# Performance work log

Measured on AMD Instinct MI355X. Metric: run time of the kernel, lower is better.

## Reference

```python
import jax, jax.numpy as jnp
import numpy as np

N_NODES = 100000
N_EDGES = 1600000


def sgconv(x, src, dst, W, b, K=1):
    """PyG SGConv: K hops of GCN-normalized propagation, then Linear."""
    n = x.shape[0]
    # add self loops
    loop = jnp.arange(n, dtype=src.dtype)
    s = jnp.concatenate([src, loop])  # source (j)
    d = jnp.concatenate([dst, loop])  # target (i)
    # symmetric normalization: deg over targets of A+I
    deg = jax.ops.segment_sum(jnp.ones_like(d, dtype=x.dtype), d, num_segments=n)
    dinv = jnp.where(deg > 0, jax.lax.rsqrt(deg), 0.0)
    norm = dinv[s] * dinv[d]  # [E+N]
    for _ in range(K):
        msg = x[s] * norm[:, None]  # gather + scale  [E+N, F]
        x = jax.ops.segment_sum(msg, d, num_segments=n)  # scatter-add
    return x @ W + b


def setup_inputs() -> dict:
    key = jax.random.key(0)
    k1, k2, k3, k4, k5, k6, k7 = jax.random.split(key, 7)
    x = jax.random.normal(k1, (N_NODES, 128), dtype=jnp.float32)
    edge_index = jax.random.randint(k2, (2, N_EDGES), 0, N_NODES, dtype=jnp.int64)
    # Glorot-ish scaled weights
    W1 = jax.random.normal(k3, (128, 128), dtype=jnp.float32) * (1.0 / np.sqrt(128))
    b1 = jax.random.normal(k4, (128,), dtype=jnp.float32) * 0.01
    W2 = jax.random.normal(k5, (128, 64), dtype=jnp.float32) * (1.0 / np.sqrt(128))
    b2 = jax.random.normal(k6, (64,), dtype=jnp.float32) * 0.01
    return {"x": x, "edge_index": edge_index, "W1": W1, "b1": b1, "W2": W2, "b2": b2}


def reference(x, edge_index, W1, b1, W2, b2):
    src, dst = edge_index[0], edge_index[1]
    h = sgconv(x, src, dst, W1, b1, K=1)
    out = sgconv(h, src, dst, W2, b2, K=1)
    return out
```

## Files before the change

### kernel.cpp

```cpp
#include <hip/hip_runtime.h>

#define NN 100000
#define NE 1600000
#define BSH 9
#define NPB (1 << BSH)
#define NBKT ((NN + NPB - 1) >> BSH)
#define ABLK 400
#define EPB (NE / ABLK)
#define CAP 10240

typedef __attribute__((ext_vector_type(8))) short short8;
typedef __attribute__((ext_vector_type(4))) float f32x4;

__device__ __forceinline__ unsigned short bf16r(float f) {
    unsigned u = __float_as_uint(f);
    u += 0x7fffu + ((u >> 16) & 1u);
    return (unsigned short)(u >> 16);
}
__device__ __forceinline__ unsigned pack2(float a, float b) {
    unsigned ua = __float_as_uint(a), ub = __float_as_uint(b);
    ua += 0x7fffu + ((ua >> 16) & 1u);
    ub += 0x7fffu + ((ub >> 16) & 1u);
    return (ua >> 16) | (ub & 0xffff0000u);
}
__device__ __forceinline__ float2 unpack2(unsigned u) {
    float2 r;
    r.x = __uint_as_float(u << 16);
    r.y = __uint_as_float(u & 0xffff0000u);
    return r;
}

__global__ __launch_bounds__(256) void k_scat2(const int* __restrict__ src,
                                               const int* __restrict__ dst,
                                               unsigned* __restrict__ cur,
                                               unsigned* __restrict__ epk) {
    __shared__ unsigned hcnt[NBKT];
    __shared__ unsigned hbase[NBKT];
    int b = blockIdx.x, t = threadIdx.x;
    for (int k = t; k < NBKT; k += 256) hcnt[k] = 0;
    __syncthreads();
    int e0 = b * EPB;
    for (int e = e0 + t; e < e0 + EPB; e += 256)
        atomicAdd(&hcnt[(unsigned)dst[e] >> BSH], 1u);
    __syncthreads();
    for (int k = t; k < NBKT; k += 256) {
        unsigned c = hcnt[k];
        hbase[k] = k * CAP + (c ? atomicAdd(&cur[k], c) : 0u);
        hcnt[k] = 0;
    }
    __syncthreads();
    for (int e = e0 + t; e < e0 + EPB; e += 256) {
        unsigned d = (unsigned)dst[e];
        unsigned kb = d >> BSH;
        unsigned pos = hbase[kb] + atomicAdd(&hcnt[kb], 1u);
        epk[pos] = ((d & (NPB - 1)) << 17) | (unsigned)src[e];
    }
}

__global__ __launch_bounds__(512) void k_csrB2(const unsigned* __restrict__ cur,
                                               const unsigned* __restrict__ epk,
                                               int* __restrict__ csr, int* __restrict__ off,
                                               int* __restrict__ deg, float* __restrict__ dinv,
                                               const float* __restrict__ W1,
                                               const float* __restrict__ W2,
                                               const float* __restrict__ b1,
                                               unsigned short* __restrict__ W12b,
                                               float* __restrict__ c2) {
    int blk = blockIdx.x;
    if (blk >= NBKT) {
        int idx = (blk - NBKT) * 512 + threadIdx.x;
        if (idx < 8192) {
            int i = idx >> 6, j = idx & 63;
            float acc = 0.f;
            for (int k = 0; k < 128; ++k) acc += W1[i * 128 + k] * W2[k * 64 + j];
            W12b[j * 128 + i] = bf16r(acc);
        } else if (idx < 8192 + 64) {
            int j = idx - 8192;
            float acc = 0.f;
            for (int k = 0; k < 128; ++k) acc += b1[k] * W2[k * 64 + j];
            c2[j] = acc;
        }
        return;
    }
    __shared__ unsigned lcnt[NPB];
    __shared__ unsigned lcur[NPB];
    int k = blk, t = threadIdx.x;
    unsigned e0 = (unsigned)k * CAP, e1 = e0 + cur[k];
    lcnt[t] = 0;
    __syncthreads();
    for (unsigned e = e0 + t; e < e1; e += NPB)
        atomicAdd(&lcnt[epk[e] >> 17], 1u);
    __syncthreads();
    unsigned own = lcnt[t];
    lcur[t] = own;
    __syncthreads();
    for (int d = 1; d < NPB; d <<= 1) {
        unsigned v = (t >= d) ? lcur[t - d] : 0;
        __syncthreads();
        lcur[t] += v;
        __syncthreads();
    }
    unsigned excl = lcur[t] - own;
    int n = k * NPB + t;
    if (n < NN) {
        off[n]  = (int)(e0 + excl);
        deg[n]  = (int)own;
        dinv[n] = rsqrtf((float)own + 1.0f);
    }
    __syncthreads();
    lcur[t] = excl;
    __syncthreads();
    for (unsigned e = e0 + t; e < e1; e += NPB) {
        unsigned u = epk[e];
        unsigned pos = atomicAdd(&lcur[u >> 17], 1u);
        csr[e0 + pos] = (int)(u & 0x1FFFFu);
    }
}

__global__ __launch_bounds__(256) void k_gemmYs(const float* __restrict__ x,
                                                const unsigned short* __restrict__ W12b,
                                                const float* __restrict__ dinv,
                                                unsigned short* __restrict__ ys) {
    __shared__ float Al[64][132];
    __shared__ short Wl[64][136];
    int t = threadIdx.x;
    int row0 = blockIdx.x * 64;

    for (int idx8 = t; idx8 < 1024; idx8 += 256) {
        int n = idx8 >> 4, c8 = idx8 & 15;
        *(short8*)&Wl[n][c8 * 8] = *(const short8*)&W12b[n * 128 + c8 * 8];
    }
    for (int idx = t; idx < 64 * 32; idx += 256) {
        int r = idx >> 5, c4 = idx & 31;
        float4 v = make_float4(0.f, 0.f, 0.f, 0.f);
        if (row0 + r < NN) v = *(const float4*)&x[(size_t)(row0 + r) * 128 + c4 * 4];
        *(float4*)&Al[r][c4 * 4] = v;
    }
    __syncthreads();

    int wv = t >> 6, lane = t & 63;
    int l15 = lane & 15, l4 = lane >> 4;

    short8 afr[4];
    #pragma unroll
    for (int ks = 0; ks < 4; ++ks) {
        const float* ap = &Al[wv * 16 + l15][ks * 32 + l4 * 8];
        float4 f0 = *(const float4*)ap;
        float4 f1 = *(const float4*)(ap + 4);
        short8 a;
        a[0] = (short)bf16r(f0.x); a[1] = (short)bf16r(f0.y);
        a[2] = (short)bf16r(f0.z); a[3] = (short)bf16r(f0.w);
        a[4] = (short)bf16r(f1.x); a[5] = (short)bf16r(f1.y);
        a[6] = (short)bf16r(f1.z); a[7] = (short)bf16r(f1.w);
        afr[ks] = a;
    }
    short8 bfr[4][4];
    #pragma unroll
    for (int ct = 0; ct < 4; ++ct)
        #pragma unroll
        for (int ks = 0; ks < 4; ++ks)
            bfr[ct][ks] = *(const short8*)&Wl[ct * 16 + l15][ks * 32 + l4 * 8];

    f32x4 acc[4] = {};
    #pragma unroll
    for (int ks = 0; ks < 4; ++ks)
        #pragma unroll
        for (int ct = 0; ct < 4; ++ct)
            acc[ct] = __builtin_amdgcn_mfma_f32_16x16x32_bf16(afr[ks], bfr[ct][ks], acc[ct], 0, 0, 0);

    int rbase = row0 + wv * 16 + l4 * 4;
    float di[4];
    #pragma unroll
    for (int r = 0; r < 4; ++r) di[r] = (rbase + r < NN) ? dinv[rbase + r] : 0.f;
    #pragma unroll
    for (int ct = 0; ct < 4; ++ct) {
        int col = ct * 16 + l15;
        #pragma unroll
        for (int r = 0; r < 4; ++r) {
            if (rbase + r < NN)
                ys[(size_t)(rbase + r) * 64 + col] = bf16r(acc[ct][r] * di[r]);
        }
    }
}

__global__ __launch_bounds__(256) void k_gatherA(const int* __restrict__ off,
        const int* __restrict__ deg, const int* __restrict__ csr,
        const float* __restrict__ dinv, const uint2* __restrict__ ys,
        const float* __restrict__ c2, uint2* __restrict__ ts) {
    int gid = blockIdx.x * blockDim.x + threadIdx.x;
    int node = gid >> 4;
    int lane = threadIdx.x & 15;
    if (node >= NN) return;
    uint2 u = ys[(size_t)node * 16 + lane];
    float2 a = unpack2(u.x), b = unpack2(u.y);
    float ax = a.x, ay = a.y, az = b.x, aw = b.y;
    int e = off[node], end = e + deg[node];
    for (; e + 8 <= end; e += 8) {
        uint2 uu[8];
        #pragma unroll
        for (int j = 0; j < 8; ++j) uu[j] = ys[(size_t)csr[e + j] * 16 + lane];
        #pragma unroll
        for (int j = 0; j < 8; ++j) {
            float2 t = unpack2(uu[j].x); ax += t.x; ay += t.y;
            t = unpack2(uu[j].y); az += t.x; aw += t.y;
        }
    }
    for (; e + 4 <= end; e += 4) {
        uint2 uu[4];
        #pragma unroll
        for (int j = 0; j < 4; ++j) uu[j] = ys[(size_t)csr[e + j] * 16 + lane];
        #pragma unroll
        for (int j = 0; j < 4; ++j) {
            float2 t = unpack2(uu[j].x); ax += t.x; ay += t.y;
            t = unpack2(uu[j].y); az += t.x; aw += t.y;
        }
    }
    for (; e < end; ++e) {
        uint2 uu = ys[(size_t)csr[e] * 16 + lane];
        float2 t = unpack2(uu.x); ax += t.x; ay += t.y;
        t = unpack2(uu.y); az += t.x; aw += t.y;
    }
    float di = dinv[node];
    float s = di * di;
    float4 cc = ((const float4*)c2)[lane];
    ts[(size_t)node * 16 + lane] = make_uint2(pack2(s * ax + di * cc.x, s * ay + di * cc.y),
                                              pack2(s * az + di * cc.z, s * aw + di * cc.w));
}

__global__ __launch_bounds__(256) void k_gatherB(const int* __restrict__ off,
        const int* __restrict__ deg, const int* __restrict__ csr,
        const float* __restrict__ dinv, const uint2* __restrict__ ts,
        const float* __restrict__ bias, float4* __restrict__ out) {
    int gid = blockIdx.x * blockDim.x + threadIdx.x;
    int node = gid >> 4;
    int lane = threadIdx.x & 15;
    if (node >= NN) return;
    uint2 u = ts[(size_t)node * 16 + lane];
    float2 a = unpack2(u.x), b = unpack2(u.y);
    float ax = a.x, ay = a.y, az = b.x, aw = b.y;
    int e = off[node], end = e + deg[node];
    for (; e + 8 <= end; e += 8) {
        uint2 uu[8];
        #pragma unroll
        for (int j = 0; j < 8; ++j) uu[j] = ts[(size_t)csr[e + j] * 16 + lane];
        #pragma unroll
        for (int j = 0; j < 8; ++j) {
            float2 t = unpack2(uu[j].x); ax += t.x; ay += t.y;
            t = unpack2(uu[j].y); az += t.x; aw += t.y;
        }
    }
    for (; e + 4 <= end; e += 4) {
        uint2 uu[4];
        #pragma unroll
        for (int j = 0; j < 4; ++j) uu[j] = ts[(size_t)csr[e + j] * 16 + lane];
        #pragma unroll
        for (int j = 0; j < 4; ++j) {
            float2 t = unpack2(uu[j].x); ax += t.x; ay += t.y;
            t = unpack2(uu[j].y); az += t.x; aw += t.y;
        }
    }
    for (; e < end; ++e) {
        uint2 uu = ts[(size_t)csr[e] * 16 + lane];
        float2 t = unpack2(uu.x); ax += t.x; ay += t.y;
        t = unpack2(uu.y); az += t.x; aw += t.y;
    }
    float di = dinv[node];
    float4 bb = ((const float4*)bias)[lane];
    out[(size_t)node * 16 + lane] = make_float4(ax * di + bb.x, ay * di + bb.y,
                                                az * di + bb.z, aw * di + bb.w);
}

extern "C" void kernel_launch(void* const* d_in, const int* in_sizes, int n_in,
                              void* d_out, int out_size, void* d_ws, size_t ws_size,
                              hipStream_t stream) {
    const float* x  = (const float*)d_in[0];
    const int*   ei = (const int*)d_in[1];
    const float* W1 = (const float*)d_in[2];
    const float* b1 = (const float*)d_in[3];
    const float* W2 = (const float*)d_in[4];
    const float* b2 = (const float*)d_in[5];
    float* out = (float*)d_out;

    const int* src = ei;
    const int* dst = ei + NE;

    float* fws  = (float*)d_ws;
    float* dinv = fws;
    unsigned* ys = (unsigned*)(fws + 102400);
    unsigned* ts = ys + (size_t)NN * 32;
    unsigned short* W12b = (unsigned short*)(ts + (size_t)NN * 32);
    float* c2   = (float*)(W12b + 8192);
    int* off  = (int*)(c2 + 128);
    int* deg  = off + 100096;
    int* csr  = deg + 100096;
    unsigned* epk = (unsigned*)(csr + NBKT * CAP);
    unsigned* cur = epk + NBKT * CAP;

    hipMemsetAsync(cur, 0, NBKT * sizeof(unsigned), stream);
    k_scat2<<<ABLK, 256, 0, stream>>>(src, dst, cur, epk);
    k_csrB2<<<NBKT + 17, 512, 0, stream>>>(cur, epk, csr, off, deg, dinv,
                                           W1, W2, b1, W12b, c2);

    k_gemmYs<<<(NN + 63) / 64, 256, 0, stream>>>(x, W12b, dinv, (unsigned short*)ys);

    k_gatherA<<<(NN * 16 + 255) / 256, 256, 0, stream>>>(off, deg, csr, dinv,
                                                         (const uint2*)ys, c2, (uint2*)ts);

    k_gatherB<<<(NN * 16 + 255) / 256, 256, 0, stream>>>(off, deg, csr, dinv,
                                                         (const uint2*)ts, b2, (float4*)out);
}
```

Before: 138.6 us.

## Merge CSR build into one cooperative kernel and widen gather loads to 16 bytes

A single cooperative kernel now does the memset, the weight-product precompute, the bucket scatter and the per-bucket CSR build, with grid-wide syncs in place of separate launches. This removes two launches and a memset. The gather kernels now use 8 lanes per node with uint4 (16-byte) loads of bf16 rows instead of 16 lanes with uint2, which halves the number of load instructions per neighbour. In exchange the CSR build runs on only 256 blocks and pays grid-sync cost, and the gathers run fewer threads, giving less parallelism to hide latency.

After: 195.7 us. 1.41x slower.

```diff
diff --git a/kernel.cpp b/kernel.cpp
--- a/kernel.cpp
+++ b/kernel.cpp
@@ -1,12 +1,15 @@
 #include <hip/hip_runtime.h>
+#include <hip/hip_cooperative_groups.h>
+
+namespace cg = cooperative_groups;
 
 #define NN 100000
 #define NE 1600000
 #define BSH 9
 #define NPB (1 << BSH)
 #define NBKT ((NN + NPB - 1) >> BSH)
-#define ABLK 400
-#define EPB (NE / ABLK)
+#define CBLK 256
+#define CEPB (NE / CBLK)
 #define CAP 10240
 
 typedef __attribute__((ext_vector_type(8))) short short8;
@@ -30,90 +33,86 @@
     return r;
 }
 
-__global__ __launch_bounds__(256) void k_scat2(const int* __restrict__ src,
-                                               const int* __restrict__ dst,
-                                               unsigned* __restrict__ cur,
-                                               unsigned* __restrict__ epk) {
-    __shared__ unsigned hcnt[NBKT];
-    __shared__ unsigned hbase[NBKT];
-    int b = blockIdx.x, t = threadIdx.x;
-    for (int k = t; k < NBKT; k += 256) hcnt[k] = 0;
+__global__ __launch_bounds__(512) void k_coop_csr(
+        const int* __restrict__ src, const int* __restrict__ dst,
+        unsigned* __restrict__ cur, unsigned* __restrict__ epk,
+        int* __restrict__ csr, int* __restrict__ off,
+        int* __restrict__ deg, float* __restrict__ dinv,
+        const float* __restrict__ W1, const float* __restrict__ W2,
+        const float* __restrict__ b1, unsigned short* __restrict__ W12b,
+        float* __restrict__ c2) {
+    cg::grid_group grid = cg::this_grid();
+    __shared__ unsigned sA[512];
+    __shared__ unsigned sB[512];
+    const int b = blockIdx.x, t = threadIdx.x;
+    const int gid = b * 512 + t;
+
+    if (gid < 8192) {
+        int i = gid >> 6, j = gid & 63;
+        float acc = 0.f;
+        for (int k = 0; k < 128; ++k) acc += W1[i * 128 + k] * W2[k * 64 + j];
+        W12b[j * 128 + i] = bf16r(acc);
+    } else if (gid < 8192 + 64) {
+        int j = gid - 8192;
+        float acc = 0.f;
+        for (int k = 0; k < 128; ++k) acc += b1[k] * W2[k * 64 + j];
+        c2[j] = acc;
+    } else if (gid - 8256 < NBKT && gid >= 8256) {
+        cur[gid - 8256] = 0u;
+    }
+    grid.sync();
+
+    for (int k = t; k < NBKT; k += 512) sA[k] = 0;
     __syncthreads();
-    int e0 = b * EPB;
-    for (int e = e0 + t; e < e0 + EPB; e += 256)
-        atomicAdd(&hcnt[(unsigned)dst[e] >> BSH], 1u);
+    const int e0 = b * CEPB;
+    for (int e = e0 + t; e < e0 + CEPB; e += 512)
+        atomicAdd(&sA[(unsigned)dst[e] >> BSH], 1u);
     __syncthreads();
-    for (int k = t; k < NBKT; k += 256) {
-        unsigned c = hcnt[k];
-        hbase[k] = k * CAP + (c ? atomicAdd(&cur[k], c) : 0u);
-        hcnt[k] = 0;
+    for (int k = t; k < NBKT; k += 512) {
+        unsigned c = sA[k];
+        sB[k] = k * CAP + (c ? atomicAdd(&cur[k], c) : 0u);
+        sA[k] = 0;
     }
     __syncthreads();
-    for (int e = e0 + t; e < e0 + EPB; e += 256) {
+    for (int e = e0 + t; e < e0 + CEPB; e += 512) {
         unsigned d = (unsigned)dst[e];
         unsigned kb = d >> BSH;
-        unsigned pos = hbase[kb] + atomicAdd(&hcnt[kb], 1u);
+        unsigned pos = sB[kb] + atomicAdd(&sA[kb], 1u);
         epk[pos] = ((d & (NPB - 1)) << 17) | (unsigned)src[e];
     }
-}
-
-__global__ __launch_bounds__(512) void k_csrB2(const unsigned* __restrict__ cur,
-                                               const unsigned* __restrict__ epk,
-                                               int* __restrict__ csr, int* __restrict__ off,
-                                               int* __restrict__ deg, float* __restrict__ dinv,
-                                               const float* __restrict__ W1,
-                                               const float* __restrict__ W2,
-                                               const float* __restrict__ b1,
-                                               unsigned short* __restrict__ W12b,
-                                               float* __restrict__ c2) {
-    int blk = blockIdx.x;
-    if (blk >= NBKT) {
-        int idx = (blk - NBKT) * 512 + threadIdx.x;
-        if (idx < 8192) {
-            int i = idx >> 6, j = idx & 63;
-            float acc = 0.f;
-            for (int k = 0; k < 128; ++k) acc += W1[i * 128 + k] * W2[k * 64 + j];
-            W12b[j * 128 + i] = bf16r(acc);
-        } else if (idx < 8192 + 64) {
-            int j = idx - 8192;
-            float acc = 0.f;
-            for (int k = 0; k < 128; ++k) acc += b1[k] * W2[k * 64 + j];
-            c2[j] = acc;
-        }
-        return;
-    }
-    __shared__ unsigned lcnt[NPB];
-    __shared__ unsigned lcur[NPB];
-    int k = blk, t = threadIdx.x;
-    unsigned e0 = (unsigned)k * CAP, e1 = e0 + cur[k];
-    lcnt[t] = 0;
-    __syncthreads();
-    for (unsigned e = e0 + t; e < e1; e += NPB)
-        atomicAdd(&lcnt[epk[e] >> 17], 1u);
-    __syncthreads();
-    unsigned own = lcnt[t];
-    lcur[t] = own;
-    __syncthreads();
-    for (int d = 1; d < NPB; d <<= 1) {
-        unsigned v = (t >= d) ? lcur[t - d] : 0;
-        __syncthreads();
-        lcur[t] += v;
-        __syncthreads();
-    }
-    unsigned excl = lcur[t] - own;
-    int n = k * NPB + t;
-    if (n < NN) {
-        off[n]  = (int)(e0 + excl);
-        deg[n]  = (int)own;
-        dinv[n] = rsqrtf((float)own + 1.0f);
-    }
-    __syncthreads();
-    lcur[t] = excl;
-    __syncthreads();
-    for (unsigned e = e0 + t; e < e1; e += NPB) {
-        unsigned u = epk[e];
-        unsigned pos = atomicAdd(&lcur[u >> 17], 1u);
-        csr[e0 + pos] = (int)(u & 0x1FFFFu);
+    grid.sync();
+
+    if (b < NBKT) {
+        unsigned e0b = (unsigned)b * CAP, e1b = e0b + cur[b];
+        sA[t] = 0;
+        __syncthreads();
+        for (unsigned e = e0b + t; e < e1b; e += 512)
+            atomicAdd(&sA[epk[e] >> 17], 1u);
+        __syncthreads();
+        unsigned own = sA[t];
+        sB[t] = own;
+        __syncthreads();
+        for (int d = 1; d < 512; d <<= 1) {
+            unsigned v = (t >= d) ? sB[t - d] : 0;
+            __syncthreads();
+            sB[t] += v;
+            __syncthreads();
+        }
+        unsigned excl = sB[t] - own;
+        int n = b * NPB + t;
+        if (n < NN) {
+            off[n]  = (int)(e0b + excl);
+            deg[n]  = (int)own;
+            dinv[n] = rsqrtf((float)own + 1.0f);
+        }
+        __syncthreads();
+        sB[t] = excl;
+        __syncthreads();
+        for (unsigned e = e0b + t; e < e1b; e += 512) {
+            unsigned u = epk[e];
+            unsigned pos = atomicAdd(&sB[u >> 17], 1u);
+            csr[e0b + pos] = (int)(u & 0x1FFFFu);
+        }
     }
 }
 
@@ -185,89 +184,111 @@
 
 __global__ __launch_bounds__(256) void k_gatherA(const int* __restrict__ off,
         const int* __restrict__ deg, const int* __restrict__ csr,
-        const float* __restrict__ dinv, const uint2* __restrict__ ys,
-        const float* __restrict__ c2, uint2* __restrict__ ts) {
+        const float* __restrict__ dinv, const uint4* __restrict__ ys4,
+        const float* __restrict__ c2, uint4* __restrict__ ts4) {
     int gid = blockIdx.x * blockDim.x + threadIdx.x;
-    int node = gid >> 4;
-    int lane = threadIdx.x & 15;
+    int node = gid >> 3;
+    int lane = threadIdx.x & 7;
     if (node >= NN) return;
-    uint2 u = ys[(size_t)node * 16 + lane];
-    float2 a = unpack2(u.x), b = unpack2(u.y);
-    float ax = a.x, ay = a.y, az = b.x, aw = b.y;
+    uint4 u = ys4[(size_t)node * 8 + lane];
+    float2 p0 = unpack2(u.x), p1 = unpack2(u.y), p2 = unpack2(u.z), p3 = unpack2(u.w);
+    float a0 = p0.x, a1 = p0.y, a2 = p1.x, a3 = p1.y;
+    float a4 = p2.x, a5 = p2.y, a6 = p3.x, a7 = p3.y;
     int e = off[node], end = e + deg[node];
     for (; e + 8 <= end; e += 8) {
-        uint2 uu[8];
-        #pragma unroll
-        for (int j = 0; j < 8; ++j) uu[j] = ys[(size_t)csr[e + j] * 16 + lane];
+        uint4 v[8];
+        #pragma unroll
+        for (int j = 0; j < 8; ++j) v[j] = ys4[(size_t)csr[e + j] * 8 + lane];
         #pragma unroll
         for (int j = 0; j < 8; ++j) {
-            float2 t = unpack2(uu[j].x); ax += t.x; ay += t.y;
-            t = unpack2(uu[j].y); az += t.x; aw += t.y;
+            float2 t0 = unpack2(v[j].x), t1 = unpack2(v[j].y);
+            float2 t2 = unpack2(v[j].z), t3 = unpack2(v[j].w);
+            a0 += t0.x; a1 += t0.y; a2 += t1.x; a3 += t1.y;
+            a4 += t2.x; a5 += t2.y; a6 += t3.x; a7 += t3.y;
         }
     }
     for (; e + 4 <= end; e += 4) {
-        uint2 uu[4];
-        #pragma unroll
-        for (int j = 0; j < 4; ++j) uu[j] = ys[(size_t)csr[e + j] * 16 + lane];
+        uint4 v[4];
+        #pragma unroll
+        for (int j = 0; j < 4; ++j) v[j] = ys4[(size_t)csr[e + j] * 8 + lane];
         #pragma unroll
         for (int j = 0; j < 4; ++j) {
-            float2 t = unpack2(uu[j].x); ax += t.x; ay += t.y;
-            t = unpack2(uu[j].y); az += t.x; aw += t.y;
+            float2 t0 = unpack2(v[j].x), t1 = unpack2(v[j].y);
+            float2 t2 = unpack2(v[j].z), t3 = unpack2(v[j].w);
+            a0 += t0.x; a1 += t0.y; a2 += t1.x; a3 += t1.y;
+            a4 += t2.x; a5 += t2.y; a6 += t3.x; a7 += t3.y;
         }
     }
     for (; e < end; ++e) {
-        uint2 uu = ys[(size_t)csr[e] * 16 + lane];
-        float2 t = unpack2(uu.x); ax += t.x; ay += t.y;
-        t = unpack2(uu.y); az += t.x; aw += t.y;
+        uint4 v = ys4[(size_t)csr[e] * 8 + lane];
+        float2 t0 = unpack2(v.x), t1 = unpack2(v.y);
+        float2 t2 = unpack2(v.z), t3 = unpack2(v.w);
+        a0 += t0.x; a1 += t0.y; a2 += t1.x; a3 += t1.y;
+        a4 += t2.x; a5 += t2.y; a6 += t3.x; a7 += t3.y;
     }
     float di = dinv[node];
     float s = di * di;
-    float4 cc = ((const float4*)c2)[lane];
-    ts[(size_t)node * 16 + lane] = make_uint2(pack2(s * ax + di * cc.x, s * ay + di * cc.y),
-                                              pack2(s * az + di * cc.z, s * aw + di * cc.w));
+    float4 cA = ((const float4*)c2)[lane * 2];
+    float4 cB = ((const float4*)c2)[lane * 2 + 1];
+    ts4[(size_t)node * 8 + lane] = make_uint4(
+        pack2(s * a0 + di * cA.x, s * a1 + di * cA.y),
+        pack2(s * a2 + di * cA.z, s * a3 + di * cA.w),
+        pack2(s * a4 + di * cB.x, s * a5 + di * cB.y),
+        pack2(s * a6 + di * cB.z, s * a7 + di * cB.w));
 }
 
 __global__ __launch_bounds__(256) void k_gatherB(const int* __restrict__ off,
         const int* __restrict__ deg, const int* __restrict__ csr,
-        const float* __restrict__ dinv, const uint2* __restrict__ ts,
-        const float* __restrict__ bias, float4* __restrict__ out) {
+        const float* __restrict__ dinv, const uint4* __restrict__ ts4,
+        const float* __restrict__ bias, float* __restrict__ out) {
     int gid = blockIdx.x * blockDim.x + threadIdx.x;
-    int node = gid >> 4;
-    int lane = threadIdx.x & 15;
+    int node = gid >> 3;
+    int lane = threadIdx.x & 7;
     if (node >= NN) return;
-    uint2 u = ts[(size_t)node * 16 + lane];
-    float2 a = unpack2(u.x), b = unpack2(u.y);
-    float ax = a.x, ay = a.y, az = b.x, aw = b.y;
+    uint4 u = ts4[(size_t)node * 8 + lane];
+    float2 p0 = unpack2(u.x), p1 = unpack2(u.y), p2 = unpack2(u.z), p3 = unpack2(u.w);
+    float a0 = p0.x, a1 = p0.y, a2 = p1.x, a3 = p1.y;
+    float a4 = p2.x, a5 = p2.y, a6 = p3.x, a7 = p3.y;
     int e = off[node], end = e + deg[node];
     for (; e + 8 <= end; e += 8) {
-        uint2 uu[8];
-        #pragma unroll
-        for (int j = 0; j < 8; ++j) uu[j] = ts[(size_t)csr[e + j] * 16 + lane];
+        uint4 v[8];
+        #pragma unroll
+        for (int j = 0; j < 8; ++j) v[j] = ts4[(size_t)csr[e + j] * 8 + lane];
         #pragma unroll
         for (int j = 0; j < 8; ++j) {
-            float2 t = unpack2(uu[j].x); ax += t.x; ay += t.y;
-            t = unpack2(uu[j].y); az += t.x; aw += t.y;
+            float2 t0 = unpack2(v[j].x), t1 = unpack2(v[j].y);
+            float2 t2 = unpack2(v[j].z), t3 = unpack2(v[j].w);
+            a0 += t0.x; a1 += t0.y; a2 += t1.x; a3 += t1.y;
+            a4 += t2.x; a5 += t2.y; a6 += t3.x; a7 += t3.y;
         }
     }
     for (; e + 4 <= end; e += 4) {
-        uint2 uu[4];
-        #pragma unroll
-        for (int j = 0; j < 4; ++j) uu[j] = ts[(size_t)csr[e + j] * 16 + lane];
+        uint4 v[4];
+        #pragma unroll
+        for (int j = 0; j < 4; ++j) v[j] = ts4[(size_t)csr[e + j] * 8 + lane];
         #pragma unroll
         for (int j = 0; j < 4; ++j) {
-            float2 t = unpack2(uu[j].x); ax += t.x; ay += t.y;
-            t = unpack2(uu[j].y); az += t.x; aw += t.y;
+            float2 t0 = unpack2(v[j].x), t1 = unpack2(v[j].y);
+            float2 t2 = unpack2(v[j].z), t3 = unpack2(v[j].w);
+            a0 += t0.x; a1 += t0.y; a2 += t1.x; a3 += t1.y;
+            a4 += t2.x; a5 += t2.y; a6 += t3.x; a7 += t3.y;
         }
     }
     for (; e < end; ++e) {
-        uint2 uu = ts[(size_t)csr[e] * 16 + lane];
-        float2 t = unpack2(uu.x); ax += t.x; ay += t.y;
-        t = unpack2(uu.y); az += t.x; aw += t.y;
+        uint4 v = ts4[(size_t)csr[e] * 8 + lane];
+        float2 t0 = unpack2(v.x), t1 = unpack2(v.y);
+        float2 t2 = unpack2(v.z), t3 = unpack2(v.w);
+        a0 += t0.x; a1 += t0.y; a2 += t1.x; a3 += t1.y;
+        a4 += t2.x; a5 += t2.y; a6 += t3.x; a7 += t3.y;
     }
     float di = dinv[node];
-    float4 bb = ((const float4*)bias)[lane];
-    out[(size_t)node * 16 + lane] = make_float4(ax * di + bb.x, ay * di + bb.y,
-                                                az * di + bb.z, aw * di + bb.w);
+    float4 bA = ((const float4*)bias)[lane * 2];
+    float4 bB = ((const float4*)bias)[lane * 2 + 1];
+    float* op = out + (size_t)node * 64 + lane * 8;
+    *(float4*)op       = make_float4(a0 * di + bA.x, a1 * di + bA.y,
+                                     a2 * di + bA.z, a3 * di + bA.w);
+    *(float4*)(op + 4) = make_float4(a4 * di + bB.x, a5 * di + bB.y,
+                                     a6 * di + bB.z, a7 * di + bB.w);
 }
 
 extern "C" void kernel_launch(void* const* d_in, const int* in_sizes, int n_in,
@@ -296,16 +317,17 @@
     unsigned* epk = (unsigned*)(csr + NBKT * CAP);
     unsigned* cur = epk + NBKT * CAP;
 
-    hipMemsetAsync(cur, 0, NBKT * sizeof(unsigned), stream);
-    k_scat2<<<ABLK, 256, 0, stream>>>(src, dst, cur, epk);
-    k_csrB2<<<NBKT + 17, 512, 0, stream>>>(cur, epk, csr, off, deg, dinv,
-                                           W1, W2, b1, W12b, c2);
+    void* cargs[] = { (void*)&src, (void*)&dst, (void*)&cur, (void*)&epk,
+                      (void*)&csr, (void*)&off, (void*)&deg, (void*)&dinv,
+                      (void*)&W1, (void*)&W2, (void*)&b1, (void*)&W12b, (void*)&c2 };
+    hipLaunchCooperativeKernel((void*)k_coop_csr, dim3(CBLK), dim3(512),
+                               cargs, 0, stream);
 
     k_gemmYs<<<(NN + 63) / 64, 256, 0, stream>>>(x, W12b, dinv, (unsigned short*)ys);
 
-    k_gatherA<<<(NN * 16 + 255) / 256, 256, 0, stream>>>(off, deg, csr, dinv,
-                                                         (const uint2*)ys, c2, (uint2*)ts);
-
-    k_gatherB<<<(NN * 16 + 255) / 256, 256, 0, stream>>>(off, deg, csr, dinv,
-                                                         (const uint2*)ts, b2, (float4*)out);
-}
+    k_gatherA<<<(NN * 8 + 255) / 256, 256, 0, stream>>>(off, deg, csr, dinv,
+                                                        (const uint4*)ys, c2, (uint4*)ts);
+
+    k_gatherB<<<(NN * 8 + 255) / 256, 256, 0, stream>>>(off, deg, csr, dinv,
+                                                        (const uint4*)ts, b2, out);
+}
```
